# Performance work log

Measured on AMD Instinct MI355X. Metric: run time of the kernel, lower is better.

## Reference

```python
import jax, jax.numpy as jnp
import numpy as np

B, S, D, H = 4, 1024, 1024, 16
HD = D // H  # head_dim = 64


def setup_inputs() -> dict:
    key = jax.random.key(0)
    ks = jax.random.split(key, 12)
    std = 1.0 / np.sqrt(D)
    inp = {
        "query": jax.random.normal(ks[0], (B, S, D), jnp.float32),
        "key": jax.random.normal(ks[1], (B, S, D), jnp.float32),
        "value": jax.random.normal(ks[2], (B, S, D), jnp.float32),
        # four Linear(embed_dim, embed_dim) layers: q, k, v, out
        "Wq": jax.random.normal(ks[3], (D, D), jnp.float32) * std,
        "bq": jnp.zeros((D,), jnp.float32),
        "Wk": jax.random.normal(ks[4], (D, D), jnp.float32) * std,
        "bk": jnp.zeros((D,), jnp.float32),
        "Wv": jax.random.normal(ks[5], (D, D), jnp.float32) * std,
        "bv": jnp.zeros((D,), jnp.float32),
        "Wo": jax.random.normal(ks[6], (D, D), jnp.float32) * std,
        "bo": jnp.zeros((D,), jnp.float32),
        # compressor: Linear(num_heads, 1)
        "Wc": jax.random.normal(ks[7], (H,), jnp.float32) / np.sqrt(H),
        "bc": jnp.zeros((), jnp.float32),
    }
    return inp


def reference(query, key, value, Wq, bq, Wk, bk, Wv, bv, Wo, bo, Wc, bc):
    b, s, d = query.shape
    h, hd = H, HD

    def proj(x, W, bias):
        # [b,s,d] @ [d,d] -> [b,h,s,hd]
        y = jnp.einsum('bsd,de->bse', x, W) + bias
        return y.reshape(b, s, h, hd).transpose(0, 2, 1, 3)

    q = proj(query, Wq, bq)
    k = proj(key, Wk, bk)
    v = proj(value, Wv, bv)

    scores = jnp.einsum('bhqd,bhkd->bhqk', q, k) / np.sqrt(hd)
    p_attn = jax.nn.softmax(scores, axis=-1)  # [b,h,s,s]; dropout is identity in eval

    x = jnp.einsum('bhqk,bhkd->bhqd', p_attn, v)
    x = x.transpose(0, 2, 1, 3).reshape(b, s, d)
    out = jnp.einsum('bsd,de->bse', x, Wo) + bo

    # head compression: Linear(num_heads, 1) over head axis -> [b,1,s,s]
    attn_c = (jnp.einsum('bhqk,h->bqk', p_attn, Wc) + bc)[:, None, :, :]
    return out, attn_c
```

## Files before the change

### kernel.cpp

```cpp
#include <hip/hip_runtime.h>
#include <hip/hip_bf16.h>

#define SS 1024
#define DD 1024
#define HH 16
#define HDh 64

typedef short bf16x8 __attribute__((ext_vector_type(8)));
typedef float f32x4 __attribute__((ext_vector_type(4)));

__device__ inline unsigned short f2bf(float f) {
    union { __hip_bfloat16 h; unsigned short u; } cv;
    cv.h = __float2bfloat16(f);
    return cv.u;
}
__device__ inline float bf2f(short u) {
    unsigned int x = ((unsigned int)(unsigned short)u) << 16;
    return __uint_as_float(x);
}

#define PIN4(a, b, c, d) asm volatile("" : "+v"(a), "+v"(b), "+v"(c), "+v"(d))

__device__ inline void gload_lds16(const unsigned short* g, unsigned short* l) {
    __builtin_amdgcn_global_load_lds(
        (const __attribute__((address_space(1))) unsigned int*)g,
        (__attribute__((address_space(3))) unsigned int*)l, 16, 0, 0);
}

__global__ __launch_bounds__(256) void prep(
    const float* __restrict__ a, const float* __restrict__ b, const float* __restrict__ c,
    unsigned short* __restrict__ oa, unsigned short* __restrict__ ob, unsigned short* __restrict__ oc,
    const float* __restrict__ Wq, const float* __restrict__ Wk,
    const float* __restrict__ Wv, const float* __restrict__ Wo,
    unsigned short* __restrict__ oq, unsigned short* __restrict__ okk,
    unsigned short* __restrict__ ov, unsigned short* __restrict__ oo)
{
    __shared__ float tile[32][33];
    int bid = blockIdx.x;
    if (bid < 4096) {
        size_t i = ((size_t)bid * 256 + threadIdx.x) * 4;
        float4 va = *(const float4*)(a + i);
        float4 vb = *(const float4*)(b + i);
        float4 vc = *(const float4*)(c + i);
        *(ushort4*)(oa + i) = make_ushort4(f2bf(va.x), f2bf(va.y), f2bf(va.z), f2bf(va.w));
        *(ushort4*)(ob + i) = make_ushort4(f2bf(vb.x), f2bf(vb.y), f2bf(vb.z), f2bf(vb.w));
        *(ushort4*)(oc + i) = make_ushort4(f2bf(vc.x), f2bf(vc.y), f2bf(vc.z), f2bf(vc.w));
    } else {
        int idx = bid - 4096;
        int z = idx >> 10;
        const float* W = z == 0 ? Wq : (z == 1 ? Wk : (z == 2 ? Wv : Wo));
        unsigned short* O = z == 0 ? oq : (z == 1 ? okk : (z == 2 ? ov : oo));
        int e0 = (idx & 31) * 32, d0 = ((idx >> 5) & 31) * 32;
        int r = threadIdx.x >> 3, c4 = (threadIdx.x & 7) * 4;
        float4 v = *(const float4*)(W + (size_t)(d0 + r) * DD + e0 + c4);
        tile[r][c4 + 0] = v.x; tile[r][c4 + 1] = v.y; tile[r][c4 + 2] = v.z; tile[r][c4 + 3] = v.w;
        __syncthreads();
        ushort4 u = make_ushort4(f2bf(tile[c4 + 0][r]), f2bf(tile[c4 + 1][r]),
                                 f2bf(tile[c4 + 2][r]), f2bf(tile[c4 + 3][r]));
        *(ushort4*)(O + (size_t)(e0 + r) * DD + d0 + c4) = u;
    }
}

__device__ inline void stage128(const unsigned short* __restrict__ A,
                                const unsigned short* __restrict__ Bt,
                                int m0, int n0, int k0,
                                unsigned short* As, unsigned short* Bs,
                                int w, int lane)
{
    int colg = (lane & 3) ^ ((lane >> 2) & 3) ^ ((lane >> 4) & 3);
#pragma unroll
    for (int i = 0; i < 4; i++) {
        int chunk = w + i * 4;
        int half = chunk >> 3;
        int c = chunk & 7;
        const unsigned short* g = (half ? Bt : A)
            + (size_t)((half ? n0 : m0) + c * 16 + (lane >> 2)) * DD + k0 + colg * 8;
        unsigned short* l = (half ? Bs : As) + c * 512 + lane * 8;
        gload_lds16(g, l);
    }
}

__device__ inline void gemm128_core(const unsigned short* __restrict__ A,
                                    const unsigned short* __restrict__ Bt,
                                    const float* __restrict__ bias,
                                    void* __restrict__ out, int mode, float oscale,
                                    int m0, int n0)
{
    __shared__ unsigned short As[2][4096];
    __shared__ unsigned short Bs[2][4096];
    int t = threadIdx.x;
    int w = t >> 6, lane = t & 63, quad = lane >> 4, l15 = lane & 15;
    int wm = w >> 1, wn = w & 1;
    int fsw = (l15 & 3) ^ ((l15 >> 2) & 3);

    f32x4 zero = {0.f, 0.f, 0.f, 0.f};
    f32x4 acc[4][4];
#pragma unroll
    for (int i = 0; i < 4; i++)
#pragma unroll
        for (int j = 0; j < 4; j++) acc[i][j] = zero;

    stage128(A, Bt, m0, n0, 0, As[0], Bs[0], w, lane);
    __syncthreads();

    int cur = 0;
    for (int k0 = 0; k0 < DD; k0 += 32) {
        if (k0 + 32 < DD)
            stage128(A, Bt, m0, n0, k0 + 32, As[cur ^ 1], Bs[cur ^ 1], w, lane);

        bf16x8 af[4], bfr[4];
#pragma unroll
        for (int mi = 0; mi < 4; mi++)
            af[mi] = *(const bf16x8*)&As[cur][(wm * 64 + mi * 16 + l15) * 32 + (quad ^ fsw) * 8];
#pragma unroll
        for (int ni = 0; ni < 4; ni++)
            bfr[ni] = *(const bf16x8*)&Bs[cur][(wn * 64 + ni * 16 + l15) * 32 + (quad ^ fsw) * 8];
#pragma unroll
        for (int mi = 0; mi < 4; mi++)
#pragma unroll
            for (int ni = 0; ni < 4; ni++)
                acc[mi][ni] = __builtin_amdgcn_mfma_f32_16x16x32_bf16(af[mi], bfr[ni], acc[mi][ni], 0, 0, 0);

        __syncthreads();
        cur ^= 1;
    }

#pragma unroll
    for (int mi = 0; mi < 4; mi++)
#pragma unroll
        for (int ni = 0; ni < 4; ni++) {
            int n = n0 + wn * 64 + ni * 16 + l15;
            float bv = bias[n];
#pragma unroll
            for (int r = 0; r < 4; r++) {
                int m = m0 + wm * 64 + mi * 16 + quad * 4 + r;
                float v = (acc[mi][ni][r] + bv) * oscale;
                if (mode == 2) {
                    ((float*)out)[(size_t)m * DD + n] = v;
                } else {
                    int bb = m >> 10, s = m & 1023, hh = n >> 6, d = n & 63;
                    size_t head = (size_t)(bb * HH + hh) << 16;
                    size_t off;
                    if (mode == 0) {
                        off = head + (((size_t)(s >> 4) * 2 + (d >> 5)) * 64
                              + ((d >> 3) & 3) * 16 + (s & 15)) * 8 + (d & 7);
                    } else {
                        off = head + (((size_t)(s >> 5) * 4 + (d >> 4)) * 64
                              + ((s >> 3) & 3) * 16 + (d & 15)) * 8 + (s & 7);
                    }
                    ((unsigned short*)out)[off] = f2bf(v);
                }
            }
        }
}

#define SCLQ 0.18033688f

__global__ __launch_bounds__(256, 3) void gemm_qkv(
    const unsigned short* __restrict__ xq, const unsigned short* __restrict__ xk,
    const unsigned short* __restrict__ xv,
    const unsigned short* __restrict__ wtq, const unsigned short* __restrict__ wtk,
    const unsigned short* __restrict__ wtv,
    const float* __restrict__ bq, const float* __restrict__ bk, const float* __restrict__ bv,
    unsigned short* __restrict__ q, unsigned short* __restrict__ k, unsigned short* __restrict__ v)
{
    int bid = blockIdx.x;
    int swz = (bid & 7) * 96 + (bid >> 3);
    int z = swz >> 8, rem = swz & 255;
    int n0 = (rem & 7) * 128, m0 = (rem >> 3) * 128;
    const unsigned short* A  = z == 0 ? xq  : (z == 1 ? xk  : xv);
    const unsigned short* Bt = z == 0 ? wtq : (z == 1 ? wtk : wtv);
    const float* bias        = z == 0 ? bq  : (z == 1 ? bk  : bv);
    void* out                = z == 0 ? (void*)q : (z == 1 ? (void*)k : (void*)v);
    gemm128_core(A, Bt, bias, out, z == 2 ? 1 : 0, z == 0 ? SCLQ : 1.0f, m0, n0);
}

__global__ __launch_bounds__(256, 3) void gemm_o(
    const unsigned short* __restrict__ x, const unsigned short* __restrict__ wto,
    const float* __restrict__ bo, float* __restrict__ out)
{
    int bid = blockIdx.x;
    int swz = (bid & 7) * 32 + (bid >> 3);
    int n0 = (swz & 7) * 128, m0 = (swz >> 3) * 128;
    gemm128_core(x, wto, bo, out, 2, 1.0f, m0, n0);
}


__global__ __launch_bounds__(256, 2) void fattn_kernel(
    const unsigned short* __restrict__ qf, const unsigned short* __restrict__ kf,
    const unsigned short* __restrict__ vf, float* __restrict__ Z,
    unsigned short* __restrict__ xat)
{
    __shared__ __align__(16) unsigned short plds[4][1280];
    int t = threadIdx.x, w = t >> 6, lane = t & 63, quad = lane >> 4, l15 = lane & 15;
    int bid = blockIdx.x;
    int swz = (bid & 7) * 64 + (bid >> 3);
    int bh = swz >> 3, m0 = (swz & 7) * 128;
    int b = bh >> 4, h = bh & 15;
    const unsigned short* qh = qf + ((size_t)bh << 16);
    const unsigned short* kh = kf + ((size_t)bh << 16);
    const unsigned short* vh = vf + ((size_t)bh << 16);

    bf16x8 qfrag[2][2];
    int s16b = (m0 >> 4) + w * 2;
#pragma unroll
    for (int mi = 0; mi < 2; mi++)
#pragma unroll
        for (int dh = 0; dh < 2; dh++)
            qfrag[mi][dh] = *(const bf16x8*)(qh + (size_t)((s16b + mi) * 2 + dh) * 512 + lane * 8);

    f32x4 zero = {0.f, 0.f, 0.f, 0.f};
    f32x4 oacc[2][4];
#pragma unroll
    for (int mi = 0; mi < 2; mi++)
#pragma unroll
        for (int ni = 0; ni < 4; ni++) oacc[mi][ni] = zero;
    float zacc[2] = {0.f, 0.f};

    bf16x8 kc[4], vc[4];
#pragma unroll
    for (int i = 0; i < 4; i++) {
        kc[i] = *(const bf16x8*)(kh + (size_t)i * 512 + lane * 8);
        vc[i] = *(const bf16x8*)(vh + (size_t)i * 512 + lane * 8);
    }

    for (int kt = 0; kt < 32; kt++) {
        int nk = kt < 31 ? kt + 1 : 31;
        bf16x8 kn[4], vn[4];
#pragma unroll
        for (int i = 0; i < 4; i++) {
            kn[i] = *(const bf16x8*)(kh + ((size_t)nk * 4 + i) * 512 + lane * 8);
            vn[i] = *(const bf16x8*)(vh + ((size_t)nk * 4 + i) * 512 + lane * 8);
        }
        PIN4(kn[0], kn[1], kn[2], kn[3]);
        PIN4(vn[0], vn[1], vn[2], vn[3]);

        f32x4 st[2][2];
#pragma unroll
        for (int si = 0; si < 2; si++)
#pragma unroll
            for (int mi = 0; mi < 2; mi++) {
                st[si][mi] = __builtin_amdgcn_mfma_f32_16x16x32_bf16(kc[si * 2 + 0], qfrag[mi][0], zero, 0, 0, 0);
                st[si][mi] = __builtin_amdgcn_mfma_f32_16x16x32_bf16(kc[si * 2 + 1], qfrag[mi][1], st[si][mi], 0, 0, 0);
            }

#pragma unroll
        for (int mi = 0; mi < 2; mi++)
#pragma unroll
            for (int si = 0; si < 2; si++) {
                float p0 = exp2f(st[si][mi][0]);
                float p1 = exp2f(st[si][mi][1]);
                float p2 = exp2f(st[si][mi][2]);
                float p3 = exp2f(st[si][mi][3]);
                zacc[mi] += (p0 + p1) + (p2 + p3);
                unsigned int pk0 = (unsigned int)f2bf(p0) | ((unsigned int)f2bf(p1) << 16);
                unsigned int pk1 = (unsigned int)f2bf(p2) | ((unsigned int)f2bf(p3) << 16);
                *(uint2*)&plds[w][(mi * 16 + l15) * 40 + si * 16 + quad * 4] = make_uint2(pk0, pk1);
            }
        bf16x8 pa[2];
#pragma unroll
        for (int mi = 0; mi < 2; mi++)
            pa[mi] = *(const bf16x8*)&plds[w][(mi * 16 + l15) * 40 + quad * 8];

#pragma unroll
        for (int mi = 0; mi < 2; mi++)
#pragma unroll
            for (int ni = 0; ni < 4; ni++)
                oacc[mi][ni] = __builtin_amdgcn_mfma_f32_16x16x32_bf16(pa[mi], vc[ni], oacc[mi][ni], 0, 0, 0);

#pragma unroll
        for (int i = 0; i < 4; i++) { kc[i] = kn[i]; vc[i] = vn[i]; }
    }

    float zt[2];
#pragma unroll
    for (int mi = 0; mi < 2; mi++) {
        float s = zacc[mi];
        s += __shfl_xor(s, 16);
        s += __shfl_xor(s, 32);
        zt[mi] = s;
        if (quad == 0)
            Z[(size_t)bh * 1024 + m0 + w * 32 + mi * 16 + l15] = s;
    }

#pragma unroll
    for (int mi = 0; mi < 2; mi++)
#pragma unroll
        for (int r = 0; r < 4; r++) {
            int qrow = quad * 4 + r;
            float iz = 1.f / __shfl(zt[mi], qrow);
            int q = m0 + w * 32 + mi * 16 + qrow;
#pragma unroll
            for (int ni = 0; ni < 4; ni++)
                xat[((size_t)(b * 1024 + q)) * 1024 + h * 64 + ni * 16 + l15] =
                    f2bf(oacc[mi][ni][r] * iz);
        }
}

__global__ __launch_bounds__(256, 3) void tail_kernel(
    const unsigned short* __restrict__ qf, const unsigned short* __restrict__ kf,
    const float* __restrict__ Z, const float* __restrict__ Wc,
    const float* __restrict__ bcp, float* __restrict__ attc,
    const unsigned short* __restrict__ xat, const unsigned short* __restrict__ wto,
    const float* __restrict__ bo, float* __restrict__ out0)
{
    if (blockIdx.x >= 512) {
        int bid2 = blockIdx.x - 512;
        int swz = (bid2 & 7) * 32 + (bid2 >> 3);
        int n0 = (swz & 7) * 128, m0 = (swz >> 3) * 128;
        gemm128_core(xat, wto, bo, out0, 2, 1.0f, m0, n0);
        return;
    }
    int t = threadIdx.x, w = t >> 6, lane = t & 63, quad = lane >> 4, l15 = lane & 15;
    int bid = blockIdx.x;
    int u = (bid & 7) * 64 + (bid >> 3);
    int kb = u & 7, qg = (u >> 3) & 15, b = u >> 7;
    int qt = qg * 4 + w;
    int q = qt * 16 + l15;
    float bc = *bcp;
    f32x4 zero = {0.f, 0.f, 0.f, 0.f};
    f32x4 acc[4][2];
#pragma unroll
    for (int kt = 0; kt < 4; kt++)
#pragma unroll
        for (int si = 0; si < 2; si++) acc[kt][si] = zero;

    for (int h = 0; h < 16; h++) {
        int bh = b * 16 + h;
        const unsigned short* qh = qf + ((size_t)bh << 16);
        const unsigned short* kh = kf + ((size_t)bh << 16);
        bf16x8 qfr0 = *(const bf16x8*)(qh + (size_t)(qt * 2 + 0) * 512 + lane * 8);
        bf16x8 qfr1 = *(const bf16x8*)(qh + (size_t)(qt * 2 + 1) * 512 + lane * 8);
        float wz = Wc[h] / Z[(size_t)bh * 1024 + q];
#pragma unroll
        for (int kt = 0; kt < 4; kt++) {
            int akt = kb * 4 + kt;
            bf16x8 kfr[4];
#pragma unroll
            for (int i = 0; i < 4; i++)
                kfr[i] = *(const bf16x8*)(kh + ((size_t)akt * 4 + i) * 512 + lane * 8);
#pragma unroll
            for (int si = 0; si < 2; si++) {
                f32x4 st = __builtin_amdgcn_mfma_f32_16x16x32_bf16(kfr[si * 2 + 0], qfr0, zero, 0, 0, 0);
                st = __builtin_amdgcn_mfma_f32_16x16x32_bf16(kfr[si * 2 + 1], qfr1, st, 0, 0, 0);
#pragma unroll
                for (int r = 0; r < 4; r++)
                    acc[kt][si][r] += wz * exp2f(st[r]);
            }
        }
    }
#pragma unroll
    for (int kt = 0; kt < 4; kt++)
#pragma unroll
        for (int si = 0; si < 2; si++) {
            float4 vv = make_float4(acc[kt][si][0] + bc, acc[kt][si][1] + bc,
                                    acc[kt][si][2] + bc, acc[kt][si][3] + bc);
            *(float4*)(attc + ((size_t)(b * 1024 + q)) * 1024 + kb * 128 + kt * 32 + si * 16 + quad * 4) = vv;
        }
}

#define LDK(f) (*(const bf16x8*)(kh + ((size_t)(f) * 64 + lane) * 8))
#define LDV(f) (*(const bf16x8*)(vh + ((size_t)(f) * 64 + lane) * 8))

__global__ __launch_bounds__(1024, 4) void attn_kernel(
    const unsigned short* __restrict__ qf, const unsigned short* __restrict__ kf,
    const unsigned short* __restrict__ vf, const float* __restrict__ Wc,
    const float* __restrict__ bcp, unsigned short* __restrict__ xout,
    float* __restrict__ attc)
{
    __shared__ float accc[16][1028];
    __shared__ unsigned short tsc[16][16][36];

    int t = threadIdx.x, w = t >> 6, lane = t & 63, quad = lane >> 4, l15 = lane & 15;
    int b = blockIdx.x >> 6, qt = blockIdx.x & 63;
    int h = w;

    for (int i = t; i < 16 * 1028; i += 1024) (&accc[0][0])[i] = 0.f;
    __syncthreads();

    const unsigned short* qh = qf + ((size_t)(b * HH + h) << 16);
    const unsigned short* kh = kf + ((size_t)(b * HH + h) << 16);
    const unsigned short* vh = vf + ((size_t)(b * HH + h) << 16);
    float wc = Wc[h], bc = *bcp;
    f32x4 zero = {0.f, 0.f, 0.f, 0.f};

    bf16x8 a0 = *(const bf16x8*)(qh + ((size_t)(qt * 2 + 0) * 64 + lane) * 8);
    bf16x8 a1 = *(const bf16x8*)(qh + ((size_t)(qt * 2 + 1) * 64 + lane) * 8);

    float rs[4] = {0.f, 0.f, 0.f, 0.f};
    bf16x8 c0 = LDK(0), c1 = LDK(1), c2 = LDK(2), c3 = LDK(3);
    PIN4(c0, c1, c2, c3);
    bf16x8 d0 = LDK(4), d1 = LDK(5), d2 = LDK(6), d3 = LDK(7);
    PIN4(d0, d1, d2, d3);
#pragma unroll 2
    for (int g = 0; g < 32; g++) {
        int gn = g < 30 ? g + 2 : 31;
        bf16x8 n0 = LDK(gn * 4 + 0), n1 = LDK(gn * 4 + 1);
        bf16x8 n2 = LDK(gn * 4 + 2), n3 = LDK(gn * 4 + 3);
        PIN4(n0, n1, n2, n3);
        f32x4 s0 = zero, s1 = zero;
        s0 = __builtin_amdgcn_mfma_f32_16x16x32_bf16(a0, c0, s0, 0, 0, 0);
        s0 = __builtin_amdgcn_mfma_f32_16x16x32_bf16(a1, c1, s0, 0, 0, 0);
        s1 = __builtin_amdgcn_mfma_f32_16x16x32_bf16(a0, c2, s1, 0, 0, 0);
        s1 = __builtin_amdgcn_mfma_f32_16x16x32_bf16(a1, c3, s1, 0, 0, 0);
#pragma unroll
        for (int r = 0; r < 4; r++) rs[r] += exp2f(s0[r]) + exp2f(s1[r]);
        c0 = d0; c1 = d1; c2 = d2; c3 = d3;
        d0 = n0; d1 = n1; d2 = n2; d3 = n3;
    }
#pragma unroll
    for (int r = 0; r < 4; r++) {
        rs[r] += __shfl_xor(rs[r], 1);
        rs[r] += __shfl_xor(rs[r], 2);
        rs[r] += __shfl_xor(rs[r], 4);
        rs[r] += __shfl_xor(rs[r], 8);
    }
    float invC[4], sC[4];
#pragma unroll
    for (int r = 0; r < 4; r++) { invC[r] = 1.f / rs[r]; sC[r] = wc * invC[r]; }

    f32x4 o0 = zero, o1 = zero, o2 = zero, o3 = zero;
    int cc0 = (2 * w) & 31;
    bf16x8 k0 = LDK(cc0 * 4 + 0), k1 = LDK(cc0 * 4 + 1);
    bf16x8 k2 = LDK(cc0 * 4 + 2), k3 = LDK(cc0 * 4 + 3);
    PIN4(k0, k1, k2, k3);
    bf16x8 v0 = LDV(cc0 * 4 + 0), v1 = LDV(cc0 * 4 + 1);
    bf16x8 v2 = LDV(cc0 * 4 + 2), v3 = LDV(cc0 * 4 + 3);
    PIN4(v0, v1, v2, v3);
#pragma unroll 2
    for (int i = 0; i < 32; i++) {
        int cc = (i + 2 * w) & 31;
        int cn = ((i + 1) + 2 * w) & 31;
        bf16x8 kn0 = LDK(cn * 4 + 0), kn1 = LDK(cn * 4 + 1);
        bf16x8 kn2 = LDK(cn * 4 + 2), kn3 = LDK(cn * 4 + 3);
        PIN4(kn0, kn1, kn2, kn3);
        bf16x8 vn0 = LDV(cn * 4 + 0), vn1 = LDV(cn * 4 + 1);
        bf16x8 vn2 = LDV(cn * 4 + 2), vn3 = LDV(cn * 4 + 3);
        PIN4(vn0, vn1, vn2, vn3);

        f32x4 s0 = zero, s1 = zero;
        s0 = __builtin_amdgcn_mfma_f32_16x16x32_bf16(a0, k0, s0, 0, 0, 0);
        s0 = __builtin_amdgcn_mfma_f32_16x16x32_bf16(a1, k1, s0, 0, 0, 0);
        s1 = __builtin_amdgcn_mfma_f32_16x16x32_bf16(a0, k2, s1, 0, 0, 0);
        s1 = __builtin_amdgcn_mfma_f32_16x16x32_bf16(a1, k3, s1, 0, 0, 0);

#pragma unroll
        for (int r = 0; r < 4; r++) {
            float p0 = exp2f(s0[r]);
            float p1 = exp2f(s1[r]);
            int row = quad * 4 + r;
            tsc[w][row][l15] = f2bf(p0);
            tsc[w][row][16 + l15] = f2bf(p1);
            atomicAdd(&accc[row][cc * 32 + l15], sC[r] * p0);
            atomicAdd(&accc[row][cc * 32 + 16 + l15], sC[r] * p1);
        }
        bf16x8 ap = *(const bf16x8*)&tsc[w][l15][quad * 8];

        o0 = __builtin_amdgcn_mfma_f32_16x16x32_bf16(ap, v0, o0, 0, 0, 0);
        o1 = __builtin_amdgcn_mfma_f32_16x16x32_bf16(ap, v1, o1, 0, 0, 0);
        o2 = __builtin_amdgcn_mfma_f32_16x16x32_bf16(ap, v2, o2, 0, 0, 0);
        o3 = __builtin_amdgcn_mfma_f32_16x16x32_bf16(ap, v3, o3, 0, 0, 0);
        k0 = kn0; k1 = kn1; k2 = kn2; k3 = kn3;
        v0 = vn0; v1 = vn1; v2 = vn2; v3 = vn3;
    }

    f32x4 oo[4] = {o0, o1, o2, o3};
#pragma unroll
    for (int j = 0; j < 4; j++)
#pragma unroll
        for (int r = 0; r < 4; r++) {
            int row = quad * 4 + r;
            xout[((size_t)(b * SS) + qt * 16 + row) * DD + h * 64 + j * 16 + l15] =
                f2bf(oo[j][r] * invC[r]);
        }

    __syncthreads();
    for (int i = t; i < 16 * 1024; i += 1024) {
        int row = i >> 10, col = i & 1023;
        attc[((size_t)b * SS + qt * 16 + row) * SS + col] = accc[row][col] + bc;
    }
}

extern "C" void kernel_launch(void* const* d_in, const int* in_sizes, int n_in,
                              void* d_out, int out_size, void* d_ws, size_t ws_size,
                              hipStream_t stream) {
    const float* query = (const float*)d_in[0];
    const float* key   = (const float*)d_in[1];
    const float* value = (const float*)d_in[2];
    const float* Wq = (const float*)d_in[3];
    const float* bq = (const float*)d_in[4];
    const float* Wk = (const float*)d_in[5];
    const float* bk = (const float*)d_in[6];
    const float* Wv = (const float*)d_in[7];
    const float* bv = (const float*)d_in[8];
    const float* Wo = (const float*)d_in[9];
    const float* bo = (const float*)d_in[10];
    const float* Wc = (const float*)d_in[11];
    const float* bc = (const float*)d_in[12];

    unsigned short* ws  = (unsigned short*)d_ws;
    unsigned short* xq  = ws;
    unsigned short* xk  = xq  + (size_t)4194304;
    unsigned short* xv  = xk  + (size_t)4194304;
    unsigned short* wtq = xv  + (size_t)4194304;
    unsigned short* wtk = wtq + (size_t)1048576;
    unsigned short* wtv = wtk + (size_t)1048576;
    unsigned short* wto = wtv + (size_t)1048576;
    unsigned short* qfb = wto + (size_t)1048576;
    unsigned short* kfb = qfb + (size_t)4194304;
    unsigned short* vfb = kfb + (size_t)4194304;
    unsigned short* xat = vfb + (size_t)4194304;

    float* out0 = (float*)d_out;
    float* attc = out0 + (size_t)4194304;

    const size_t base_bytes = 67108864;
    const size_t z_bytes = 262144;
    bool fast = ws_size >= base_bytes + z_bytes;

    hipLaunchKernelGGL(prep, dim3(8192), dim3(256), 0, stream,
                       query, key, value, xq, xk, xv,
                       Wq, Wk, Wv, Wo, wtq, wtk, wtv, wto);
    hipLaunchKernelGGL(gemm_qkv, dim3(768), dim3(256), 0, stream,
                       xq, xk, xv, wtq, wtk, wtv, bq, bk, bv, qfb, kfb, vfb);

    if (fast) {
        float* Zbuf = (float*)((char*)d_ws + base_bytes);
        hipLaunchKernelGGL(fattn_kernel, dim3(512), dim3(256), 0, stream,
                           qfb, kfb, vfb, Zbuf, xat);
        hipLaunchKernelGGL(tail_kernel, dim3(768), dim3(256), 0, stream,
                           qfb, kfb, Zbuf, Wc, bc, attc,
                           xat, wto, bo, out0);
    } else {
        hipLaunchKernelGGL(attn_kernel, dim3(256), dim3(1024), 0, stream,
                           qfb, kfb, vfb, Wc, bc, xat, attc);
        hipLaunchKernelGGL(gemm_o, dim3(256), dim3(256), 0, stream,
                           xat, wto, bo, out0);
    }
}
```

Measured before the change: 243.3 us.

## Rework GEMM staging, widen fattn blocks, stage K tiles in LDS for tail

The GEMM core drops its double-buffered, XOR-swizzled LDS staging and uses a single buffer with a sync on each side of every K step. The flash-attention kernel moves to 512 threads with 8 waves, each owning 16 query rows instead of 32. The tail kernel now prefetches per-head K tiles into double-buffered LDS and precomputes the Wc/Z weights up front. These aim to raise occupancy and K reuse, but the GEMM loses load/compute overlap and may suffer LDS bank conflicts without the swizzle.

```diff
diff --git a/kernel.cpp b/kernel.cpp
--- a/kernel.cpp
+++ b/kernel.cpp
@@ -61,37 +61,17 @@
     }
 }
 
-__device__ inline void stage128(const unsigned short* __restrict__ A,
-                                const unsigned short* __restrict__ Bt,
-                                int m0, int n0, int k0,
-                                unsigned short* As, unsigned short* Bs,
-                                int w, int lane)
-{
-    int colg = (lane & 3) ^ ((lane >> 2) & 3) ^ ((lane >> 4) & 3);
-#pragma unroll
-    for (int i = 0; i < 4; i++) {
-        int chunk = w + i * 4;
-        int half = chunk >> 3;
-        int c = chunk & 7;
-        const unsigned short* g = (half ? Bt : A)
-            + (size_t)((half ? n0 : m0) + c * 16 + (lane >> 2)) * DD + k0 + colg * 8;
-        unsigned short* l = (half ? Bs : As) + c * 512 + lane * 8;
-        gload_lds16(g, l);
-    }
-}
-
 __device__ inline void gemm128_core(const unsigned short* __restrict__ A,
                                     const unsigned short* __restrict__ Bt,
                                     const float* __restrict__ bias,
                                     void* __restrict__ out, int mode, float oscale,
                                     int m0, int n0)
 {
-    __shared__ unsigned short As[2][4096];
-    __shared__ unsigned short Bs[2][4096];
+    __shared__ unsigned short As[128 * 32];
+    __shared__ unsigned short Bs[128 * 32];
     int t = threadIdx.x;
     int w = t >> 6, lane = t & 63, quad = lane >> 4, l15 = lane & 15;
     int wm = w >> 1, wn = w & 1;
-    int fsw = (l15 & 3) ^ ((l15 >> 2) & 3);
 
     f32x4 zero = {0.f, 0.f, 0.f, 0.f};
     f32x4 acc[4][4];
@@ -100,29 +80,31 @@
 #pragma unroll
         for (int j = 0; j < 4; j++) acc[i][j] = zero;
 
-    stage128(A, Bt, m0, n0, 0, As[0], Bs[0], w, lane);
-    __syncthreads();
-
-    int cur = 0;
     for (int k0 = 0; k0 < DD; k0 += 32) {
-        if (k0 + 32 < DD)
-            stage128(A, Bt, m0, n0, k0 + 32, As[cur ^ 1], Bs[cur ^ 1], w, lane);
-
+        __syncthreads();
+#pragma unroll
+        for (int i = 0; i < 4; i++) {
+            int chunk = w + i * 4;
+            int half = chunk >> 3;
+            int c = chunk & 7;
+            const unsigned short* g = (half ? Bt : A)
+                + (size_t)((half ? n0 : m0) + c * 16 + (lane >> 2)) * DD + k0 + (lane & 3) * 8;
+            unsigned short* l = (half ? Bs : As) + c * 512 + lane * 8;
+            gload_lds16(g, l);
+        }
+        __syncthreads();
         bf16x8 af[4], bfr[4];
 #pragma unroll
         for (int mi = 0; mi < 4; mi++)
-            af[mi] = *(const bf16x8*)&As[cur][(wm * 64 + mi * 16 + l15) * 32 + (quad ^ fsw) * 8];
+            af[mi] = *(const bf16x8*)&As[(wm * 64 + mi * 16 + l15) * 32 + quad * 8];
 #pragma unroll
         for (int ni = 0; ni < 4; ni++)
-            bfr[ni] = *(const bf16x8*)&Bs[cur][(wn * 64 + ni * 16 + l15) * 32 + (quad ^ fsw) * 8];
+            bfr[ni] = *(const bf16x8*)&Bs[(wn * 64 + ni * 16 + l15) * 32 + quad * 8];
 #pragma unroll
         for (int mi = 0; mi < 4; mi++)
 #pragma unroll
             for (int ni = 0; ni < 4; ni++)
                 acc[mi][ni] = __builtin_amdgcn_mfma_f32_16x16x32_bf16(af[mi], bfr[ni], acc[mi][ni], 0, 0, 0);
-
-        __syncthreads();
-        cur ^= 1;
     }
 
 #pragma unroll
@@ -186,12 +168,12 @@
 }
 
 
-__global__ __launch_bounds__(256, 2) void fattn_kernel(
+__global__ __launch_bounds__(512, 4) void fattn_kernel(
     const unsigned short* __restrict__ qf, const unsigned short* __restrict__ kf,
     const unsigned short* __restrict__ vf, float* __restrict__ Z,
     unsigned short* __restrict__ xat)
 {
-    __shared__ __align__(16) unsigned short plds[4][1280];
+    __shared__ __align__(16) unsigned short plds[8][640];
     int t = threadIdx.x, w = t >> 6, lane = t & 63, quad = lane >> 4, l15 = lane & 15;
     int bid = blockIdx.x;
     int swz = (bid & 7) * 64 + (bid >> 3);
@@ -201,21 +183,17 @@
     const unsigned short* kh = kf + ((size_t)bh << 16);
     const unsigned short* vh = vf + ((size_t)bh << 16);
 
-    bf16x8 qfrag[2][2];
-    int s16b = (m0 >> 4) + w * 2;
-#pragma unroll
-    for (int mi = 0; mi < 2; mi++)
-#pragma unroll
-        for (int dh = 0; dh < 2; dh++)
-            qfrag[mi][dh] = *(const bf16x8*)(qh + (size_t)((s16b + mi) * 2 + dh) * 512 + lane * 8);
+    bf16x8 qfrag[2];
+    int s16b = (m0 >> 4) + w;
+#pragma unroll
+    for (int dh = 0; dh < 2; dh++)
+        qfrag[dh] = *(const bf16x8*)(qh + (size_t)(s16b * 2 + dh) * 512 + lane * 8);
 
     f32x4 zero = {0.f, 0.f, 0.f, 0.f};
-    f32x4 oacc[2][4];
-#pragma unroll
-    for (int mi = 0; mi < 2; mi++)
-#pragma unroll
-        for (int ni = 0; ni < 4; ni++) oacc[mi][ni] = zero;
-    float zacc[2] = {0.f, 0.f};
+    f32x4 oacc[4];
+#pragma unroll
+    for (int ni = 0; ni < 4; ni++) oacc[ni] = zero;
+    float zacc = 0.f;
 
     bf16x8 kc[4], vc[4];
 #pragma unroll
@@ -235,66 +213,50 @@
         PIN4(kn[0], kn[1], kn[2], kn[3]);
         PIN4(vn[0], vn[1], vn[2], vn[3]);
 
-        f32x4 st[2][2];
-#pragma unroll
-        for (int si = 0; si < 2; si++)
-#pragma unroll
-            for (int mi = 0; mi < 2; mi++) {
-                st[si][mi] = __builtin_amdgcn_mfma_f32_16x16x32_bf16(kc[si * 2 + 0], qfrag[mi][0], zero, 0, 0, 0);
-                st[si][mi] = __builtin_amdgcn_mfma_f32_16x16x32_bf16(kc[si * 2 + 1], qfrag[mi][1], st[si][mi], 0, 0, 0);
-            }
-
-#pragma unroll
-        for (int mi = 0; mi < 2; mi++)
-#pragma unroll
-            for (int si = 0; si < 2; si++) {
-                float p0 = exp2f(st[si][mi][0]);
-                float p1 = exp2f(st[si][mi][1]);
-                float p2 = exp2f(st[si][mi][2]);
-                float p3 = exp2f(st[si][mi][3]);
-                zacc[mi] += (p0 + p1) + (p2 + p3);
-                unsigned int pk0 = (unsigned int)f2bf(p0) | ((unsigned int)f2bf(p1) << 16);
-                unsigned int pk1 = (unsigned int)f2bf(p2) | ((unsigned int)f2bf(p3) << 16);
-                *(uint2*)&plds[w][(mi * 16 + l15) * 40 + si * 16 + quad * 4] = make_uint2(pk0, pk1);
-            }
-        bf16x8 pa[2];
-#pragma unroll
-        for (int mi = 0; mi < 2; mi++)
-            pa[mi] = *(const bf16x8*)&plds[w][(mi * 16 + l15) * 40 + quad * 8];
-
-#pragma unroll
-        for (int mi = 0; mi < 2; mi++)
-#pragma unroll
-            for (int ni = 0; ni < 4; ni++)
-                oacc[mi][ni] = __builtin_amdgcn_mfma_f32_16x16x32_bf16(pa[mi], vc[ni], oacc[mi][ni], 0, 0, 0);
+        f32x4 st[2];
+#pragma unroll
+        for (int si = 0; si < 2; si++) {
+            st[si] = __builtin_amdgcn_mfma_f32_16x16x32_bf16(kc[si * 2 + 0], qfrag[0], zero, 0, 0, 0);
+            st[si] = __builtin_amdgcn_mfma_f32_16x16x32_bf16(kc[si * 2 + 1], qfrag[1], st[si], 0, 0, 0);
+        }
+
+#pragma unroll
+        for (int si = 0; si < 2; si++) {
+            float p0 = exp2f(st[si][0]);
+            float p1 = exp2f(st[si][1]);
+            float p2 = exp2f(st[si][2]);
+            float p3 = exp2f(st[si][3]);
+            zacc += (p0 + p1) + (p2 + p3);
+            unsigned int pk0 = (unsigned int)f2bf(p0) | ((unsigned int)f2bf(p1) << 16);
+            unsigned int pk1 = (unsigned int)f2bf(p2) | ((unsigned int)f2bf(p3) << 16);
+            *(uint2*)&plds[w][l15 * 40 + si * 16 + quad * 4] = make_uint2(pk0, pk1);
+        }
+        bf16x8 pa = *(const bf16x8*)&plds[w][l15 * 40 + quad * 8];
+
+#pragma unroll
+        for (int ni = 0; ni < 4; ni++)
+            oacc[ni] = __builtin_amdgcn_mfma_f32_16x16x32_bf16(pa, vc[ni], oacc[ni], 0, 0, 0);
 
 #pragma unroll
         for (int i = 0; i < 4; i++) { kc[i] = kn[i]; vc[i] = vn[i]; }
     }
 
-    float zt[2];
-#pragma unroll
-    for (int mi = 0; mi < 2; mi++) {
-        float s = zacc[mi];
-        s += __shfl_xor(s, 16);
-        s += __shfl_xor(s, 32);
-        zt[mi] = s;
-        if (quad == 0)
-            Z[(size_t)bh * 1024 + m0 + w * 32 + mi * 16 + l15] = s;
-    }
-
-#pragma unroll
-    for (int mi = 0; mi < 2; mi++)
-#pragma unroll
-        for (int r = 0; r < 4; r++) {
-            int qrow = quad * 4 + r;
-            float iz = 1.f / __shfl(zt[mi], qrow);
-            int q = m0 + w * 32 + mi * 16 + qrow;
-#pragma unroll
-            for (int ni = 0; ni < 4; ni++)
-                xat[((size_t)(b * 1024 + q)) * 1024 + h * 64 + ni * 16 + l15] =
-                    f2bf(oacc[mi][ni][r] * iz);
-        }
+    float zt = zacc;
+    zt += __shfl_xor(zt, 16);
+    zt += __shfl_xor(zt, 32);
+    if (quad == 0)
+        Z[(size_t)bh * 1024 + m0 + w * 16 + l15] = zt;
+
+#pragma unroll
+    for (int r = 0; r < 4; r++) {
+        int qrow = quad * 4 + r;
+        float iz = 1.f / __shfl(zt, qrow);
+        int q = m0 + w * 16 + qrow;
+#pragma unroll
+        for (int ni = 0; ni < 4; ni++)
+            xat[((size_t)(b * 1024 + q)) * 1024 + h * 64 + ni * 16 + l15] =
+                f2bf(oacc[ni][r] * iz);
+    }
 }
 
 __global__ __launch_bounds__(256, 3) void tail_kernel(
@@ -311,6 +273,7 @@
         gemm128_core(xat, wto, bo, out0, 2, 1.0f, m0, n0);
         return;
     }
+    __shared__ unsigned short ks[2][8192];
     int t = threadIdx.x, w = t >> 6, lane = t & 63, quad = lane >> 4, l15 = lane & 15;
     int bid = blockIdx.x;
     int u = (bid & 7) * 64 + (bid >> 3);
@@ -325,20 +288,42 @@
 #pragma unroll
         for (int si = 0; si < 2; si++) acc[kt][si] = zero;
 
+    float wzv[16];
+#pragma unroll
+    for (int h = 0; h < 16; h++)
+        wzv[h] = Wc[h] / Z[(size_t)(b * 16 + h) * 1024 + q];
+
+    {
+        const unsigned short* src = kf + ((size_t)(b * 16) << 16) + (size_t)(kb * 16) * 512;
+#pragma unroll
+        for (int i = 0; i < 4; i++) {
+            int c = w + i * 4;
+            gload_lds16(src + (size_t)c * 512 + lane * 8, ks[0] + c * 512 + lane * 8);
+        }
+    }
+    __syncthreads();
+
+    int cb = 0;
     for (int h = 0; h < 16; h++) {
         int bh = b * 16 + h;
         const unsigned short* qh = qf + ((size_t)bh << 16);
-        const unsigned short* kh = kf + ((size_t)bh << 16);
         bf16x8 qfr0 = *(const bf16x8*)(qh + (size_t)(qt * 2 + 0) * 512 + lane * 8);
         bf16x8 qfr1 = *(const bf16x8*)(qh + (size_t)(qt * 2 + 1) * 512 + lane * 8);
-        float wz = Wc[h] / Z[(size_t)bh * 1024 + q];
+        if (h < 15) {
+            const unsigned short* src = kf + ((size_t)(bh + 1) << 16) + (size_t)(kb * 16) * 512;
+#pragma unroll
+            for (int i = 0; i < 4; i++) {
+                int c = w + i * 4;
+                gload_lds16(src + (size_t)c * 512 + lane * 8, ks[cb ^ 1] + c * 512 + lane * 8);
+            }
+        }
+        float wz = wzv[h];
 #pragma unroll
         for (int kt = 0; kt < 4; kt++) {
-            int akt = kb * 4 + kt;
             bf16x8 kfr[4];
 #pragma unroll
             for (int i = 0; i < 4; i++)
-                kfr[i] = *(const bf16x8*)(kh + ((size_t)akt * 4 + i) * 512 + lane * 8);
+                kfr[i] = *(const bf16x8*)&ks[cb][(size_t)(kt * 4 + i) * 512 + lane * 8];
 #pragma unroll
             for (int si = 0; si < 2; si++) {
                 f32x4 st = __builtin_amdgcn_mfma_f32_16x16x32_bf16(kfr[si * 2 + 0], qfr0, zero, 0, 0, 0);
@@ -348,6 +333,8 @@
                     acc[kt][si][r] += wz * exp2f(st[r]);
             }
         }
+        __syncthreads();
+        cb ^= 1;
     }
 #pragma unroll
     for (int kt = 0; kt < 4; kt++)
@@ -526,7 +513,7 @@
 
     if (fast) {
         float* Zbuf = (float*)((char*)d_ws + base_bytes);
-        hipLaunchKernelGGL(fattn_kernel, dim3(512), dim3(256), 0, stream,
+        hipLaunchKernelGGL(fattn_kernel, dim3(512), dim3(512), 0, stream,
                            qfb, kfb, vfb, Zbuf, xat);
         hipLaunchKernelGGL(tail_kernel, dim3(768), dim3(256), 0, stream,
                            qfb, kfb, Zbuf, Wc, bc, attc,
```

Result: no change. 239.3 us (-1.6%).
